# Kernel tuning notes

Measured on AMD Instinct MI355X. Metric: run time of the kernel, lower is better.

The kernel has to match this reference:

```python
import jax, jax.numpy as jnp
import numpy as np

B = 4; IN_CH = 256; HEAD_CH = 64; NUM_CLS = 3; H = 128; W = 128
NH = 4; KEY = 16; VAL = 16; OUT_CH = 2
VX = 0.1 * 8; VY = 0.1 * 8  # voxel_size[:2] * out_size_factor
DW = 1.6; DL = 3.9; STRIDE = 1
C_CTR = (HEAD_CH + 2 + NUM_CLS) * 9      # 621
C_COR = (HEAD_CH + 2 + NUM_CLS * 4) * 8  # 624
C_FG = (HEAD_CH + 2 + NUM_CLS) * 9       # 621


def _sampler_points():
    offs = np.arange(-STRIDE, STRIDE + 1, STRIDE, dtype=np.float32)
    oy, ox = np.meshgrid(offs, offs, indexing='ij')
    ctr = np.stack([ox, oy], 0).reshape(2, 9)  # pixel offsets
    cx = np.array([-DW/2, -DW/2, DW/2, DW/2, DL/2, -DL/2, DL/2, -DL/2], np.float32) / VX
    cy = np.array([DL/2, -DL/2, DL/2, -DL/2, -DW/2, -DW/2, DW/2, DW/2], np.float32) / VY
    # faithful to torch: stack(dim=1) -> [8,2] then .view(2,8) (row-major reinterpret)
    cor = np.stack([cx, cy], 1).reshape(2, 8)
    r = max(DW, DL)
    fx = np.array([-r/3, -r/3, -r/3, 0, 0, 0, r/3, r/3, r/3], np.float32) / VX
    fy = np.array([-r/3, 0, r/3, -r/3, 0, r/3, -r/3, 0, r/3], np.float32) / VY
    fg = np.stack([fx, fy], 1).reshape(2, 9)
    return jnp.asarray(ctr), jnp.asarray(cor), jnp.asarray(fg)


def _raw_grid():
    gx = jnp.arange(W, dtype=jnp.float32) + 0.5
    gy = jnp.arange(H, dtype=jnp.float32) + 0.5
    return jnp.stack([jnp.broadcast_to(gx[None, :], (H, W)),
                      jnp.broadcast_to(gy[:, None], (H, W))], 0)  # [2,H,W]


def _conv3x3(x, w, b):
    y = jax.lax.conv_general_dilated(x, w, (1, 1), 'SAME',
                                     dimension_numbers=('NCHW', 'OIHW', 'NCHW'))
    return y + b[None, :, None, None]


def _cbr3(x, w, b, s, t):  # conv3x3 + inference-mode BN (folded scale/shift) + relu
    return jax.nn.relu(_conv3x3(x, w, b) * s[None, :, None, None] + t[None, :, None, None])


def _cbr1(x, w, b, s, t):  # per-head 1x1 conv + BN + relu, w: [NH,O,C], x: [B,C,H,W]
    y = jnp.einsum('noc,bchw->nbohw', w, x) + b[:, None, :, None, None]
    return jax.nn.relu(y * s[:, None, :, None, None] + t[:, None, :, None, None])


def _sample(feats, grids):
    # feats [B,C,H,W]; grids [2,n,H,W] pixel coords. Matches F.grid_sample
    # (bilinear, zeros padding, align_corners=False): sample at pixel coord g-0.5.
    n = grids.shape[1]
    geo = jnp.stack([grids[0] / W, grids[1] / H], 0)  # recover_coords, [2,n,H,W]
    gx, gy = grids[0] - 0.5, grids[1] - 0.5
    x0f = jnp.floor(gx); y0f = jnp.floor(gy)
    dx, dy = gx - x0f, gy - y0f
    x0 = x0f.astype(jnp.int32); y0 = y0f.astype(jnp.int32)
    flat = feats.reshape(B, -1, H * W)

    def gather(xc, yc, wgt):
        valid = ((xc >= 0) & (xc < W) & (yc >= 0) & (yc < H)).astype(feats.dtype) * wgt
        idx = jnp.clip(yc, 0, H - 1) * W + jnp.clip(xc, 0, W - 1)
        v = jnp.take(flat, idx.reshape(-1), axis=2).reshape(B, -1, n, H, W)
        return v * valid[None, None]

    s = (gather(x0, y0, (1 - dx) * (1 - dy)) + gather(x0 + 1, y0, dx * (1 - dy))
         + gather(x0, y0 + 1, (1 - dx) * dy) + gather(x0 + 1, y0 + 1, dx * dy))
    geo_b = jnp.broadcast_to(geo[None], (B,) + geo.shape)
    out = jnp.concatenate([s, geo_b], axis=1)  # [B,C+2,n,H,W]
    return out.reshape(B, -1, H, W)           # channel index = c*n + p, as torch .view


def _forward(base_feats, cc_w, cc_b, cc_s, cc_t, ch_w, ch_b,
             oc_w, oc_b, oc_s, oc_t, oh_w, oh_b,
             fc_w, fc_b, fc_s, fc_t, fh_w, fh_b,
             q_w, q_b, q_s, q_t,
             ck_w, ck_b, ck_s, ck_t, cv_w, cv_b, cv_s, cv_t,
             kk_w, kk_b, kk_s, kk_t, kv_w, kv_b, kv_s, kv_t,
             fk_w, fk_b, fk_s, fk_t, fv_w, fv_b, fv_s, fv_t,
             p1_w, p1_b, p1_s, p1_t, p2_w, p2_b):
    center_feat = _cbr3(base_feats, cc_w, cc_b, cc_s, cc_t)
    center_map = _conv3x3(center_feat, ch_w, ch_b)
    corner_feat = _cbr3(base_feats, oc_w, oc_b, oc_s, oc_t)
    corner_map = _conv3x3(corner_feat, oh_w, oh_b)
    fg_feat = _cbr3(base_feats, fc_w, fc_b, fc_s, fc_t)
    fg_map = _conv3x3(fg_feat, fh_w, fh_b)

    ctr_pts, cor_pts, fg_pts = _sampler_points()
    raw = _raw_grid()
    g_ctr = raw[:, None] + ctr_pts[:, :, None, None]  # [2,9,H,W]
    g_cor = raw[:, None] + cor_pts[:, :, None, None]  # [2,8,H,W]
    g_fg = raw[:, None] + fg_pts[:, :, None, None]    # [2,9,H,W]

    cs = _sample(jnp.concatenate([center_feat, center_map], 1), g_ctr)  # [B,621,H,W]
    os_ = _sample(jnp.concatenate([corner_feat, corner_map], 1), g_cor)  # [B,624,H,W]
    fs = _sample(jnp.concatenate([fg_feat, fg_map], 1), g_fg)            # [B,621,H,W]

    q = _cbr1(base_feats, q_w, q_b, q_s, q_t)  # [NH,B,KEY,H,W]
    ck = _cbr1(cs, ck_w, ck_b, ck_s, ck_t); cv = _cbr1(cs, cv_w, cv_b, cv_s, cv_t)
    ok = _cbr1(os_, kk_w, kk_b, kk_s, kk_t); ov = _cbr1(os_, kv_w, kv_b, kv_s, kv_t)
    fk = _cbr1(fs, fk_w, fk_b, fk_s, fk_t); fv = _cbr1(fs, fv_w, fv_b, fv_s, fv_t)

    logits = jnp.stack([(q * ck).sum(2), (q * ok).sum(2), (q * fk).sum(2)], axis=2)  # [NH,B,3,H,W]
    attw = jax.nn.softmax(logits, axis=2)
    vals = jnp.stack([cv, ov, fv], axis=2)          # [NH,B,3,VAL,H,W]
    att = (attw[:, :, :, None] * vals).sum(2)       # [NH,B,VAL,H,W]

    # predict: 1x1 conv over cat([base_feats, att]) + BN + relu, then 1x1 to out_ch
    h1 = (jnp.einsum('noc,bchw->nbohw', p1_w[:, :, :IN_CH], base_feats)
          + jnp.einsum('nov,nbvhw->nbohw', p1_w[:, :, IN_CH:], att)
          + p1_b[:, None, :, None, None])
    h1 = jax.nn.relu(h1 * p1_s[:, None, :, None, None] + p1_t[:, None, :, None, None])
    pred = jnp.einsum('npo,nbohw->nbphw', p2_w, h1) + p2_b[:, None, :, None, None]
    heads = jnp.moveaxis(pred, 0, 1).reshape(B, NH * OUT_CH, H, W)
    return jnp.concatenate([center_map, corner_map, fg_map, heads], axis=1)  # [B,26,H,W]


def setup_inputs() -> dict:
    ks = iter(jax.random.split(jax.random.key(0), 80))

    def rn(shape, s=0.05):
        return jax.random.normal(next(ks), shape, jnp.float32) * s

    d = {"base_feats": jax.random.normal(next(ks), (B, IN_CH, H, W), jnp.float32)}
    for conv, head, hc in (("cc", "ch", NUM_CLS), ("oc", "oh", NUM_CLS * 4), ("fc", "fh", NUM_CLS)):
        d[conv + "_w"] = rn((HEAD_CH, IN_CH, 3, 3)); d[conv + "_b"] = rn((HEAD_CH,))
        d[conv + "_s"] = 1.0 + rn((HEAD_CH,)); d[conv + "_t"] = rn((HEAD_CH,))
        d[head + "_w"] = rn((hc, HEAD_CH, 3, 3)); d[head + "_b"] = jnp.full((hc,), -2.19, jnp.float32)
    d["q_w"] = rn((NH, KEY, IN_CH)); d["q_b"] = rn((NH, KEY))
    d["q_s"] = 1.0 + rn((NH, KEY)); d["q_t"] = rn((NH, KEY))
    for name, cin, cout in (("ck", C_CTR, KEY), ("cv", C_CTR, VAL), ("kk", C_COR, KEY),
                            ("kv", C_COR, VAL), ("fk", C_FG, KEY), ("fv", C_FG, VAL)):
        d[name + "_w"] = rn((NH, cout, cin)); d[name + "_b"] = rn((NH, cout))
        d[name + "_s"] = 1.0 + rn((NH, cout)); d[name + "_t"] = rn((NH, cout))
    d["p1_w"] = rn((NH, HEAD_CH, IN_CH + VAL)); d["p1_b"] = rn((NH, HEAD_CH))
    d["p1_s"] = 1.0 + rn((NH, HEAD_CH)); d["p1_t"] = rn((NH, HEAD_CH))
    d["p2_w"] = rn((NH, OUT_CH, HEAD_CH)); d["p2_b"] = jnp.full((NH, OUT_CH), -2.19, jnp.float32)
    return d


def reference(base_feats, cc_w, cc_b, cc_s, cc_t, ch_w, ch_b,
              oc_w, oc_b, oc_s, oc_t, oh_w, oh_b,
              fc_w, fc_b, fc_s, fc_t, fh_w, fh_b,
              q_w, q_b, q_s, q_t,
              ck_w, ck_b, ck_s, ck_t, cv_w, cv_b, cv_s, cv_t,
              kk_w, kk_b, kk_s, kk_t, kv_w, kv_b, kv_s, kv_t,
              fk_w, fk_b, fk_s, fk_t, fv_w, fv_b, fv_s, fv_t,
              p1_w, p1_b, p1_s, p1_t, p2_w, p2_b):
    return _forward(base_feats, cc_w, cc_b, cc_s, cc_t, ch_w, ch_b,
                    oc_w, oc_b, oc_s, oc_t, oh_w, oh_b,
                    fc_w, fc_b, fc_s, fc_t, fh_w, fh_b,
                    q_w, q_b, q_s, q_t,
                    ck_w, ck_b, ck_s, ck_t, cv_w, cv_b, cv_s, cv_t,
                    kk_w, kk_b, kk_s, kk_t, kv_w, kv_b, kv_s, kv_t,
                    fk_w, fk_b, fk_s, fk_t, fv_w, fv_b, fv_s, fv_t,
                    p1_w, p1_b, p1_s, p1_t, p2_w, p2_b)
```

## Files before the change

### kernel.cpp

```cpp
#include <hip/hip_runtime.h>
#include <hip/hip_bf16.h>
#include <math.h>


#define HW 16384
#define WIMG 128

typedef unsigned short ushortT;
typedef __attribute__((ext_vector_type(8))) short short8;
typedef __attribute__((ext_vector_type(4))) float floatx4;
typedef __attribute__((ext_vector_type(4))) unsigned uintx4;

constexpr size_t OFF_KV    = 16777216;
constexpr size_t OFF_A16   = 29360128;
constexpr size_t OFF_B16   = 38012928;
constexpr size_t OFF_CWT   = 46057216;
constexpr size_t OFF_CB    = OFF_CWT + 221184;
constexpr size_t OFF_HWT   = OFF_CB + 192;
constexpr size_t OFF_QWT   = OFF_HWT + 13824;
constexpr size_t OFF_QB    = OFF_QWT + 8192;
constexpr size_t OFF_KVW   = OFF_QB + 64;
constexpr size_t OFF_GEO   = OFF_KVW + 266240;
constexpr size_t OFF_P1WT  = OFF_GEO + 1152;
constexpr size_t OFF_P1B   = OFF_P1WT + 40960;

struct P53 { const float* p[53]; };

__device__ inline ushortT f2bf(float f) {
    unsigned u = __float_as_uint(f);
    unsigned r = (u + 0x7FFFu + ((u >> 16) & 1u)) >> 16;
    return (ushortT)r;
}
__device__ inline unsigned packbf(float a, float b) {
    return (unsigned)f2bf(a) | ((unsigned)f2bf(b) << 16);
}
__device__ inline float bf2f(ushortT u) {
    return __uint_as_float((unsigned)u << 16);
}

typedef __attribute__((address_space(3))) ushortT lds_us;
typedef __attribute__((address_space(1))) const ushortT glb_us;
__device__ inline void gload_lds16(const ushortT* g, ushortT* ldsbase) {
    __builtin_amdgcn_global_load_lds((glb_us*)g, (lds_us*)ldsbase, 16, 0, 0);
}

__device__ const float c_ox[3][9] = {
    {-1.f, 0.f, 1.f, -1.f, 0.f, 1.f, -1.f, 0.f, 1.f},
    {-1.f, 2.4375f, -1.f, -2.4375f, 1.f, 2.4375f, 1.f, -2.4375f, 0.f},
    {-1.625f, -1.625f, -1.625f, 0.f, -1.625f, 1.625f, 0.f, -1.625f, 0.f}};
__device__ const float c_oy[3][9] = {
    {-1.f, -1.f, -1.f, 0.f, 0.f, 0.f, 1.f, 1.f, 1.f},
    {2.4375f, -1.f, -2.4375f, -1.f, 2.4375f, 1.f, -2.4375f, 1.f, 0.f},
    {0.f, 0.f, 1.625f, 1.625f, -1.625f, 1.625f, 0.f, 1.625f, 1.625f}};

__device__ const int tapX_cor[16] = {-1,-1, 2, 3,-1,-1,-3,-2, 1, 1, 2, 3, 1, 1,-3,-2};
__device__ const int tapY_cor[16] = { 2, 3,-1,-1,-3,-2,-1,-1, 2, 3, 1, 1,-3,-2, 1, 1};
__device__ const int tapR_cor[16] = { 4, 5, 2, 2, 0, 1, 2, 2, 4, 5, 3, 3, 0, 1, 3, 3};

__device__ inline float cornw(float off, int X) {
    float f = floorf(off);
    float d = off - f;
    int fi = (int)f;
    return (X == fi) ? (1.f - d) : (X == fi + 1) ? d : 0.f;
}

__global__ __launch_bounds__(256) void setup_kernel(P53 ptrs, float* __restrict__ ws,
                                                    const float* __restrict__ base,
                                                    ushortT* __restrict__ a16,
                                                    ushortT* __restrict__ b16) {
    int i = blockIdx.x * 256 + threadIdx.x;
    const float* const* p = ptrs.p;
    if (i < 1102464) {
        if (i < 442368) {
            int tap = i / 49152, r = i % 49152;
            int g = r / 1536, r2 = r % 1536;
            int M = r2 >> 3, j = r2 & 7;
            int br = M >> 6, oc = M & 63, ic = g * 8 + j;
            float v = p[1 + 6 * br][(oc * 256 + ic) * 9 + tap] * p[3 + 6 * br][oc];
            ((ushortT*)(ws + OFF_CWT))[i] = f2bf(v);
            return;
        }
        i -= 442368;
        if (i < 192) {
            int br = i >> 6, oc = i & 63;
            ws[OFF_CB + i] = p[2 + 6 * br][oc] * p[3 + 6 * br][oc] + p[4 + 6 * br][oc];
            return;
        }
        i -= 192;
        if (i < 27648) {
            int j = i & 7, m = (i >> 3) & 15, u = (i >> 7) % 72, br = i / 9216;
            int cnt = (br == 1) ? 12 : 3;
            int t = u >> 3, g = u & 7, ic = g * 8 + j;
            const float* hw = (br == 0) ? p[5] : (br == 1) ? p[11] : p[17];
            float v = (m < cnt) ? hw[(m * 64 + ic) * 9 + t] : 0.f;
            ((ushortT*)(ws + OFF_HWT))[i] = f2bf(v);
            return;
        }
        i -= 27648;
        if (i < 16384) {
            int j = i & 7, m = (i >> 3) & 63, sg = i >> 9;
            int k = (sg >> 2) * 32 + (sg & 3) * 8 + j;
            ((ushortT*)(ws + OFF_QWT))[i] = f2bf(p[19][m * 256 + k] * p[21][m]);
            return;
        }
        i -= 16384;
        if (i < 64) { ws[OFF_QB + i] = p[20][i] * p[21][i] + p[22][i]; return; }
        i -= 64;
        if (i < 532480) {
            int br, NQ, NTAP, n, C, i2;
            if (i < 110592)      { br = 0; NQ = 3; NTAP = 9;  n = 9; C = 67; i2 = i; }
            else if (i < 274432) { br = 1; NQ = 4; NTAP = 16; n = 8; C = 76; i2 = i - 110592; }
            else                 { br = 2; NQ = 7; NTAP = 25; n = 9; C = 67; i2 = i - 274432; }
            int gsz = NQ * 4096;
            int g = i2 / gsz, r = i2 % gsz;
            int q = r >> 12, r2 = r & 4095;
            int sub = r2 >> 10, m = (r2 >> 3) & 127, j = r2 & 7;
            int t = q * 4 + sub, c = g * 8 + j;
            float v = 0.f;
            if (t < NTAP && c < C) {
                int X, Y;
                if (br == 0)      { X = t % 3 - 1; Y = t / 3 - 1; }
                else if (br == 1) { X = tapX_cor[t]; Y = tapY_cor[t]; }
                else              { X = t % 5 - 2; Y = t / 5 - 2; }
                const float* wsrc = (m < 64) ? p[23 + 8 * br] : p[27 + 8 * br];
                int mo = (m < 64) ? m : m - 64;
                float sc = (m < 64) ? p[25 + 8 * br][mo] : p[29 + 8 * br][mo];
                int Cn = (C + 2) * n;
                float s = 0.f;
                for (int pp = 0; pp < n; ++pp) {
                    float ww = cornw(c_ox[br][pp], X) * cornw(c_oy[br][pp], Y);
                    if (ww != 0.f) s += ww * wsrc[mo * Cn + c * n + pp];
                }
                v = s * sc;
            }
            ((ushortT*)(ws + OFF_KVW))[i] = f2bf(v);
            return;
        }
        i -= 532480;
        if (i < 1152) {
            int br = i / 384, rem = i % 384, which = rem >> 7, m = rem & 127;
            int n = (br == 1) ? 8 : 9, C = (br == 1) ? 76 : 67, Cn = (C + 2) * n;
            const float* wsrc = (m < 64) ? p[23 + 8 * br] : p[27 + 8 * br];
            int mo = (m < 64) ? m : m - 64;
            float sc = (m < 64) ? p[25 + 8 * br][mo] : p[29 + 8 * br][mo];
            float bb = (m < 64) ? p[24 + 8 * br][mo] : p[28 + 8 * br][mo];
            float tt = (m < 64) ? p[26 + 8 * br][mo] : p[30 + 8 * br][mo];
            float v = 0.f;
            if (which == 0) {
                for (int pp = 0; pp < n; ++pp) v += wsrc[mo * Cn + C * n + pp];
                v *= sc;
            } else if (which == 1) {
                for (int pp = 0; pp < n; ++pp) v += wsrc[mo * Cn + (C + 1) * n + pp];
                v *= sc;
            } else {
                for (int pp = 0; pp < n; ++pp)
                    v += wsrc[mo * Cn + C * n + pp] * c_ox[br][pp]
                       + wsrc[mo * Cn + (C + 1) * n + pp] * c_oy[br][pp];
                v = v * sc * 0.0078125f + bb * sc + tt;
            }
            ws[OFF_GEO + br * 384 + which * 128 + m] = v;
            return;
        }
        i -= 1152;
        if (i < 81920) {
            int j = i & 7, M = (i >> 3) & 255, sg = i >> 11;
            int k = (sg >> 2) * 32 + (sg & 3) * 8 + j;
            int nh = M >> 6, oc = M & 63;
            float sc = p[49][nh * 64 + oc];
            float v;
            if (k < 256) v = p[47][(nh * 64 + oc) * 272 + k] * sc;
            else {
                int k2 = k - 256, nh2 = k2 >> 4, va = k2 & 15;
                v = (nh2 == nh) ? p[47][(nh * 64 + oc) * 272 + 256 + va] * sc : 0.f;
            }
            ((ushortT*)(ws + OFF_P1WT))[i] = f2bf(v);
            return;
        }
        i -= 81920;
        if (i < 256) { ws[OFF_P1B + i] = p[48][i] * p[49][i] + p[50][i]; }
        return;
    }
    int idx = i - 1102464;
    if (idx < 4 * 32 * 130 * 130) {
        int col = idx % 130, t = idx / 130;
        int row = t % 130; t /= 130;
        int icg = t & 31, b = t >> 5;
        int h = row - 1, w = col - 1;
        unsigned wds[4] = {0u, 0u, 0u, 0u};
        if ((unsigned)h < 128u && (unsigned)w < 128u) {
            const float* s = base + (size_t)(b * 256 + icg * 8) * HW + h * WIMG + w;
            #pragma unroll
            for (int jp = 0; jp < 4; ++jp)
                wds[jp] = packbf(s[(size_t)(2 * jp) * HW], s[(size_t)(2 * jp + 1) * HW]);
        }
        unsigned* d = (unsigned*)(a16 + (size_t)idx * 8);
        d[0] = wds[0]; d[1] = wds[1]; d[2] = wds[2]; d[3] = wds[3];
        return;
    }
    idx -= 4 * 32 * 130 * 130;
    if (idx < 4 * 28 * 134 * 134) {
        int col = idx % 134, row = (idx / 134) % 134;
        if (row < 3 || row >= 131 || col < 3 || col >= 131) {
            unsigned* d = (unsigned*)(b16 + (size_t)idx * 8);
            d[0] = 0u; d[1] = 0u; d[2] = 0u; d[3] = 0u;
        }
    }
}

__global__ __launch_bounds__(256) void conv_base_mfma(
    const ushortT* __restrict__ a16, const ushortT* __restrict__ wA,
    const float* __restrict__ cb, ushortT* __restrict__ b16)
{
    const int wv = threadIdx.x >> 6, lane = threadIdx.x & 63;
    const int sub = lane >> 4, ln = lane & 15;
    const int xh = blockIdx.x, h = blockIdx.y, b = blockIdx.z;
    const int x0 = xh * 64;
    __shared__ __align__(16) ushortT sbuf[2][792 * 8];

    floatx4 acc[3][4];
    #pragma unroll
    for (int mt = 0; mt < 3; ++mt)
        #pragma unroll
        for (int nt = 0; nt < 4; ++nt)
            #pragma unroll
            for (int r = 0; r < 4; ++r) acc[mt][nt][r] = 0.f;

    const int wbase = threadIdx.x & ~63;
    auto stage = [&](int s, int buf) {
        #pragma unroll
        for (int it = 0; it < 4; ++it) {
            int idx = threadIdx.x + it * 256;
            if (idx < 792) {
                int col = idx % 66, t2 = idx / 66;
                int r = t2 % 3, icg = t2 / 3;
                const ushortT* g = a16 +
                    (((size_t)(b * 32 + s * 4 + icg) * 130 + (h + r)) * 130 + (x0 + col)) * 8;
                gload_lds16(g, &sbuf[buf][(size_t)(it * 256 + wbase) * 8]);
            }
        }
    };
    stage(0, 0);
    for (int s = 0; s < 8; ++s) {
        __syncthreads();
        if (s < 7) stage(s + 1, (s + 1) & 1);
        const ushortT* sb = sbuf[s & 1];
        #pragma unroll
        for (int tap = 0; tap < 9; ++tap) {
            const int ky = tap / 3, kx = tap % 3;
            short8 Bf[4];
            #pragma unroll
            for (int nt = 0; nt < 4; ++nt) {
                int c = nt * 16 + ln + kx;
                Bf[nt] = *(const short8*)(sb + ((sub * 3 + ky) * 66 + c) * 8);
            }
            const int g = s * 4 + sub;
            short8 Af[3];
            #pragma unroll
            for (int mt = 0; mt < 3; ++mt) {
                int m = wv * 48 + mt * 16 + ln;
                Af[mt] = *(const short8*)(wA + (((size_t)tap * 32 + g) * 192 + m) * 8);
            }
            #pragma unroll
            for (int mt = 0; mt < 3; ++mt)
                #pragma unroll
                for (int nt = 0; nt < 4; ++nt)
                    acc[mt][nt] = __builtin_amdgcn_mfma_f32_16x16x32_bf16(
                        Af[mt], Bf[nt], acc[mt][nt], 0, 0, 0);
        }
    }
    #pragma unroll
    for (int mt = 0; mt < 3; ++mt) {
        int ocq = wv * 48 + mt * 16 + sub * 4;
        #pragma unroll
        for (int nt = 0; nt < 4; ++nt) {
            int px = x0 + nt * 16 + ln;
            float v0 = fmaxf(acc[mt][nt][0] + cb[ocq + 0], 0.f);
            float v1 = fmaxf(acc[mt][nt][1] + cb[ocq + 1], 0.f);
            float v2 = fmaxf(acc[mt][nt][2] + cb[ocq + 2], 0.f);
            float v3 = fmaxf(acc[mt][nt][3] + cb[ocq + 3], 0.f);
            unsigned lo = packbf(v0, v1), hi = packbf(v2, v3);
            unsigned plo = (unsigned)__shfl_down((int)lo, 16);
            unsigned phi = (unsigned)__shfl_down((int)hi, 16);
            if (!(sub & 1)) {
                int br = ocq >> 6, oc = ocq & 63;
                int grp = ((br == 0) ? 0 : (br == 1) ? 9 : 19) + (oc >> 3);
                uintx4 w = {lo, hi, plo, phi};
                *(uintx4*)(b16 +
                    (((size_t)(b * 28 + grp) * 134 + (h + 3)) * 134 + (px + 3)) * 8) = w;
            }
        }
    }
}

__global__ __launch_bounds__(256) void conv_head_mfma(
    const ushortT* __restrict__ b16c, const ushortT* __restrict__ wH,
    const float* __restrict__ chb, const float* __restrict__ ohb,
    const float* __restrict__ fhb, float* __restrict__ out,
    ushortT* __restrict__ b16)
{
    const int wv = threadIdx.x >> 6, lane = threadIdx.x & 63;
    const int sub = lane >> 4, ln = lane & 15;
    const int h = blockIdx.x;
    const int br = blockIdx.y % 3, b = blockIdx.y / 3;
    const int cnt = (br == 1) ? 12 : 3;
    const int mapb = (br == 0) ? 0 : (br == 1) ? 3 : 15;
    const int grpb = (br == 0) ? 0 : (br == 1) ? 9 : 19;
    const float* bias = (br == 0) ? chb : (br == 1) ? ohb : fhb;
    __shared__ __align__(16) ushortT sbuf[8 * 3 * 130 * 8];
    const int wbase = threadIdx.x & ~63;

    for (int it = 0; it < 13; ++it) {
        int idx = threadIdx.x + it * 256;
        if (idx < 3120) {
            int col = idx % 130, t2 = idx / 130;
            int r = t2 % 3, g = t2 / 3;
            const ushortT* gp = b16c +
                (((size_t)(b * 28 + grpb + g) * 134 + (h + r + 2)) * 134 + (col + 2)) * 8;
            gload_lds16(gp, sbuf + (size_t)(it * 256 + wbase) * 8);
        }
    }
    __syncthreads();

    floatx4 acc[2];
    #pragma unroll
    for (int nt = 0; nt < 2; ++nt)
        #pragma unroll
        for (int r = 0; r < 4; ++r) acc[nt][r] = 0.f;
    #pragma unroll
    for (int k = 0; k < 18; ++k) {
        int u = k * 4 + sub;
        int t = u >> 3, g = u & 7;
        int dxv = t % 3 - 1, ry = t / 3;
        short8 Af = *(const short8*)(wH + ((size_t)(br * 72 + u) * 16 + ln) * 8);
        #pragma unroll
        for (int nt = 0; nt < 2; ++nt) {
            int c = wv * 32 + nt * 16 + ln + dxv + 1;
            short8 Bf = *(const short8*)(sbuf + ((g * 3 + ry) * 130 + c) * 8);
            acc[nt] = __builtin_amdgcn_mfma_f32_16x16x32_bf16(Af, Bf, acc[nt], 0, 0, 0);
        }
    }
    #pragma unroll
    for (int nt = 0; nt < 2; ++nt) {
        int px = wv * 32 + nt * 16 + ln;
        #pragma unroll
        for (int r = 0; r < 4; ++r) {
            int m = sub * 4 + r;
            if (m < cnt) {
                float v = acc[nt][r] + bias[m];
                out[((size_t)b * 26 + mapb + m) * HW + h * WIMG + px] = v;
                int grp = grpb + 8 + (m >> 3), j = m & 7;
                b16[(((size_t)(b * 28 + grp) * 134 + (h + 3)) * 134 + (px + 3)) * 8 + j]
                    = f2bf(v);
            }
        }
    }
}

template<int BRV>
__global__ __launch_bounds__(256, 6) void kv_grp(
    const ushortT* __restrict__ b16, const ushortT* __restrict__ kvw,
    const float* __restrict__ geob, ushortT* __restrict__ kvout)
{
    constexpr int NG    = (BRV == 0) ? 9  : (BRV == 1) ? 10 : 9;
    constexpr int NTAP  = (BRV == 0) ? 9  : (BRV == 1) ? 16 : 25;
    constexpr int NQ    = (BRV == 0) ? 3  : (BRV == 1) ? 4  : 7;
    constexpr int ROWS  = (BRV == 0) ? 3  : (BRV == 1) ? 6  : 5;
    constexpr int COLS  = (BRV == 0) ? 66 : (BRV == 1) ? 70 : 68;
    constexpr int XMIN  = (BRV == 0) ? -1 : (BRV == 1) ? -3 : -2;
    constexpr int UBASE = (BRV == 0) ? 0  : (BRV == 1) ? 9  : 19;
    constexpr int NEL   = ROWS * COLS;
    constexpr int NIT   = (NEL + 255) / 256;
    constexpr int WBASE = (BRV == 0) ? 0 : (BRV == 1) ? 110592 : 274432;

    const int lane = threadIdx.x & 63, wv = threadIdx.x >> 6;
    const int sub = lane >> 4, ln = lane & 15;
    const int mw = wv >> 1, nw = wv & 1;
    const int x0 = blockIdx.x * 64, h = blockIdx.y;
    const int b = blockIdx.z;

    __shared__ __align__(16) ushortT sbuf[2][NEL * 8];
    const int wbase = threadIdx.x & ~63;
    const int thrB = (nw * 32 + ln) * 16;

    int boff[NQ];
    #pragma unroll
    for (int q = 0; q < NQ; ++q) {
        int t = q * 4 + sub;
        int dxv, ry;
        if (t >= NTAP)          { dxv = -XMIN; ry = 0; }
        else if (BRV == 0)      { dxv = t % 3 - 1; ry = t / 3; }
        else if (BRV == 1)      { dxv = tapX_cor[t]; ry = tapR_cor[t]; }
        else                    { dxv = t % 5 - 2; ry = t / 5; }
        boff[q] = (ry * COLS + (dxv - XMIN)) * 16 + thrB;
    }

    auto stage = [&](int g, int buf) {
        #pragma unroll
        for (int it = 0; it < NIT; ++it) {
            int idx = threadIdx.x + it * 256;
            if (idx < NEL) {
                int rw = idx / COLS, col = idx % COLS;
                int dy = (BRV == 1) ? ((rw < 3) ? rw - 3 : rw - 2) : (rw - ROWS / 2);
                const ushortT* gp = b16 +
                    (((size_t)(b * 28 + UBASE + g) * 134 + (h + dy + 3)) * 134
                     + (x0 + col + XMIN + 3)) * 8;
                gload_lds16(gp, &sbuf[buf][(size_t)(it * 256 + wbase) * 8]);
            }
        }
    };

    floatx4 acc[4][2];
    #pragma unroll
    for (int mt = 0; mt < 4; ++mt)
        #pragma unroll
        for (int nt = 0; nt < 2; ++nt)
            #pragma unroll
            for (int r = 0; r < 4; ++r) acc[mt][nt][r] = 0.f;

    const ushortT* wp0 = kvw + WBASE + (size_t)sub * 1024 + (mw * 64 + ln) * 8;

    stage(0, 0);
    __syncthreads();
    int cur = 0;
    for (int g = 0; g < NG; ++g) {
        const char* sb8 = (const char*)sbuf[cur];
        const ushortT* wg = wp0 + (size_t)g * (NQ * 4096);
        short8 A0[4], B0[2], A1[4], B1[2];
        auto ldf = [&](int q, short8 A[4], short8 B[2]) {
            const ushortT* wp = wg + (size_t)q * 4096;
            #pragma unroll
            for (int mt = 0; mt < 4; ++mt)
                A[mt] = *(const short8*)(wp + mt * 128);
            int bb = boff[q];
            #pragma unroll
            for (int nt = 0; nt < 2; ++nt)
                B[nt] = *(const short8*)(sb8 + bb + nt * 256);
        };
        auto dom = [&](short8 A[4], short8 B[2]) {
            #pragma unroll
            for (int mt = 0; mt < 4; ++mt)
                #pragma unroll
                for (int nt = 0; nt < 2; ++nt)
                    acc[mt][nt] = __builtin_amdgcn_mfma_f32_16x16x32_bf16(
                        A[mt], B[nt], acc[mt][nt], 0, 0, 0);
        };
        ldf(0, A0, B0);
        if (g + 1 < NG) stage(g + 1, cur ^ 1);
        #pragma unroll
        for (int q = 0; q < NQ; q += 2) {
            bool h1 = (q + 1 < NQ);
            if (h1) ldf(q + 1, A1, B1);
            dom(A0, B0);
            if (q + 2 < NQ) ldf(q + 2, A0, B0);
            if (h1) dom(A1, B1);
        }
        __syncthreads();
        cur ^= 1;
    }

    const float* geo = geob + BRV * 384;
    const float fy = (h + 0.5f) * 0.0078125f;
    #pragma unroll
    for (int mt = 0; mt < 4; ++mt)
        #pragma unroll
        for (int nt = 0; nt < 2; ++nt) {
            int px = x0 + nw * 32 + nt * 16 + ln;
            float fx = (px + 0.5f) * 0.0078125f;
            #pragma unroll
            for (int r = 0; r < 4; ++r) {
                int Mi = mw * 64 + mt * 16 + sub * 4 + r;
                float v = acc[mt][nt][r] + geo[Mi] * fx + geo[128 + Mi] * fy + geo[256 + Mi];
                kvout[((size_t)(BRV * 4 + b) * 128 + Mi) * HW + h * WIMG + px] =
                    f2bf(fmaxf(v, 0.f));
            }
        }
}

__global__ __launch_bounds__(256) void attn_pred_mfma(
    float* __restrict__ ws, const float* __restrict__ p2w,
    const float* __restrict__ p2b, float* __restrict__ out)
{
    const int wv = threadIdx.x >> 6, lane = threadIdx.x & 63;
    const int sub = lane >> 4, ln = lane & 15;
    const int px0 = blockIdx.x * 64, b = blockIdx.y;
    const ushortT* wP1 = (const ushortT*)(ws + OFF_P1WT);
    const ushortT* wQ  = (const ushortT*)(ws + OFF_QWT);
    const ushortT* a16 = (const ushortT*)(ws + OFF_A16);
    const ushortT* kv = (const ushortT*)(ws + OFF_KV);
    const float* p1b = ws + OFF_P1B;
    const float* qb  = ws + OFF_QB;
    __shared__ __align__(16) ushortT xbuf[40 * 64 * 8];
    __shared__ __align__(16) ushortT qld[64 * 64];

    const int mypx = threadIdx.x & 63, nh = threadIdx.x >> 6;
    const int gpx = px0 + mypx, hh = gpx >> 7, ww = gpx & 127;
    #pragma unroll
    for (int g2 = 0; g2 < 8; ++g2) {
        int g = nh * 8 + g2;
        const ushortT* gp = a16 +
            (((size_t)(b * 32 + g) * 130 + (hh + 1)) * 130 + (ww + 1)) * 8;
        gload_lds16(gp, xbuf + (size_t)g * 64 * 8);
    }
    __syncthreads();

    {
        floatx4 qacc[4];
        #pragma unroll
        for (int nt = 0; nt < 4; ++nt)
            #pragma unroll
            for (int r = 0; r < 4; ++r) qacc[nt][r] = 0.f;
        #pragma unroll
        for (int kk = 0; kk < 8; ++kk) {
            short8 Af = *(const short8*)(wQ + (((kk * 4 + sub) * 64) + wv * 16 + ln) * 8);
            #pragma unroll
            for (int nt = 0; nt < 4; ++nt) {
                short8 Bf = *(const short8*)(xbuf + (((kk * 4 + sub) * 64) + nt * 16 + ln) * 8);
                qacc[nt] = __builtin_amdgcn_mfma_f32_16x16x32_bf16(Af, Bf, qacc[nt], 0, 0, 0);
            }
        }
        #pragma unroll
        for (int nt = 0; nt < 4; ++nt)
            #pragma unroll
            for (int r = 0; r < 4; ++r) {
                int row = wv * 16 + sub * 4 + r;
                qld[row * 64 + nt * 16 + ln] = f2bf(fmaxf(qacc[nt][r] + qb[row], 0.f));
            }
    }
    __syncthreads();

    {
        float l[3];
        #pragma unroll
        for (int br = 0; br < 3; ++br) {
            float s = 0.f;
            #pragma unroll
            for (int ko = 0; ko < 16; ++ko)
                s = fmaf(bf2f(qld[(nh * 16 + ko) * 64 + mypx]),
                         bf2f(kv[(size_t)((br * 4 + b) * 128 + nh * 16 + ko) * HW + gpx]), s);
            l[br] = s;
        }
        float m = fmaxf(l[0], fmaxf(l[1], l[2]));
        float e0 = __expf(l[0] - m), e1 = __expf(l[1] - m), e2 = __expf(l[2] - m);
        float inv = 1.f / (e0 + e1 + e2);
        float aw0 = e0 * inv, aw1 = e1 * inv, aw2 = e2 * inv;
        #pragma unroll
        for (int vap = 0; vap < 8; ++vap) {
            int va0 = vap * 2, va1 = vap * 2 + 1;
            float a0 =
                aw0 * bf2f(kv[(size_t)((0 * 4 + b) * 128 + 64 + nh * 16 + va0) * HW + gpx]) +
                aw1 * bf2f(kv[(size_t)((1 * 4 + b) * 128 + 64 + nh * 16 + va0) * HW + gpx]) +
                aw2 * bf2f(kv[(size_t)((2 * 4 + b) * 128 + 64 + nh * 16 + va0) * HW + gpx]);
            float a1 =
                aw0 * bf2f(kv[(size_t)((0 * 4 + b) * 128 + 64 + nh * 16 + va1) * HW + gpx]) +
                aw1 * bf2f(kv[(size_t)((1 * 4 + b) * 128 + 64 + nh * 16 + va1) * HW + gpx]) +
                aw2 * bf2f(kv[(size_t)((2 * 4 + b) * 128 + 64 + nh * 16 + va1) * HW + gpx]);
            int g = 32 + nh * 2 + (vap >> 2), wo = vap & 3;
            ((unsigned*)xbuf)[(g * 64 + mypx) * 4 + wo] = packbf(a0, a1);
        }
    }
    __syncthreads();

    floatx4 acc[4][4];
    #pragma unroll
    for (int mt = 0; mt < 4; ++mt)
        #pragma unroll
        for (int nt = 0; nt < 4; ++nt)
            #pragma unroll
            for (int r = 0; r < 4; ++r) acc[mt][nt][r] = 0.f;
    #pragma unroll
    for (int kk = 0; kk < 10; ++kk) {
        short8 Bf[4];
        #pragma unroll
        for (int nt = 0; nt < 4; ++nt)
            Bf[nt] = *(const short8*)(xbuf + (((kk * 4 + sub) * 64) + nt * 16 + ln) * 8);
        #pragma unroll
        for (int mt = 0; mt < 4; ++mt) {
            short8 Af = *(const short8*)(wP1 +
                (((size_t)(kk * 4 + sub) * 256) + wv * 64 + mt * 16 + ln) * 8);
            #pragma unroll
            for (int nt = 0; nt < 4; ++nt)
                acc[mt][nt] = __builtin_amdgcn_mfma_f32_16x16x32_bf16(Af, Bf[nt], acc[mt][nt], 0, 0, 0);
        }
    }

    float po0[4] = {0.f, 0.f, 0.f, 0.f}, po1[4] = {0.f, 0.f, 0.f, 0.f};
    #pragma unroll
    for (int mt = 0; mt < 4; ++mt)
        #pragma unroll
        for (int r = 0; r < 4; ++r) {
            int oc = mt * 16 + sub * 4 + r;
            float bias = p1b[wv * 64 + oc];
            float w0 = p2w[(wv * 2 + 0) * 64 + oc];
            float w1 = p2w[(wv * 2 + 1) * 64 + oc];
            #pragma unroll
            for (int nt = 0; nt < 4; ++nt) {
                float hv = fmaxf(acc[mt][nt][r] + bias, 0.f);
                po0[nt] = fmaf(w0, hv, po0[nt]);
                po1[nt] = fmaf(w1, hv, po1[nt]);
            }
        }
    #pragma unroll
    for (int nt = 0; nt < 4; ++nt) {
        po0[nt] += __shfl_xor(po0[nt], 16);
        po0[nt] += __shfl_xor(po0[nt], 32);
        po1[nt] += __shfl_xor(po1[nt], 16);
        po1[nt] += __shfl_xor(po1[nt], 32);
    }
    if (sub == 0) {
        #pragma unroll
        for (int nt = 0; nt < 4; ++nt) {
            int px = px0 + nt * 16 + ln;
            out[((size_t)b * 26 + 18 + wv * 2 + 0) * HW + px] = po0[nt] + p2b[wv * 2 + 0];
            out[((size_t)b * 26 + 18 + wv * 2 + 1) * HW + px] = po1[nt] + p2b[wv * 2 + 1];
        }
    }
}

extern "C" void kernel_launch(void* const* d_in, const int* in_sizes, int n_in,
                              void* d_out, int out_size, void* d_ws, size_t ws_size,
                              hipStream_t stream) {
    (void)in_sizes; (void)n_in; (void)out_size; (void)ws_size;
    float* ws  = (float*)d_ws;
    float* out = (float*)d_out;
    const float* base = (const float*)d_in[0];
    P53 ptrs;
    for (int i = 0; i < 53; ++i) ptrs.p[i] = (const float*)d_in[i];

    ushortT* a16 = (ushortT*)(ws + OFF_A16);
    ushortT* b16 = (ushortT*)(ws + OFF_B16);
    ushortT* kvb = (ushortT*)(ws + OFF_KV);
    const ushortT* kvw = (const ushortT*)(ws + OFF_KVW);

    setup_kernel<<<20613, 256, 0, stream>>>(ptrs, ws, base, a16, b16);
    conv_base_mfma<<<dim3(2, 128, 4), 256, 0, stream>>>(
        a16, (const ushortT*)(ws + OFF_CWT), ws + OFF_CB, b16);
    conv_head_mfma<<<dim3(128, 12), 256, 0, stream>>>(
        b16, (const ushortT*)(ws + OFF_HWT),
        (const float*)d_in[6], (const float*)d_in[12], (const float*)d_in[18],
        out, b16);
    kv_grp<0><<<dim3(2, 128, 4), 256, 0, stream>>>(b16, kvw, ws + OFF_GEO, kvb);
    kv_grp<1><<<dim3(2, 128, 4), 256, 0, stream>>>(b16, kvw, ws + OFF_GEO, kvb);
    kv_grp<2><<<dim3(2, 128, 4), 256, 0, stream>>>(b16, kvw, ws + OFF_GEO, kvb);
    attn_pred_mfma<<<dim3(256, 4), 256, 0, stream>>>(ws, (const float*)d_in[51],
                                                     (const float*)d_in[52], out);
}
```

Before: 460.4 us.

## Merge three kv_grp launches into one kernel and halve conv_head tile width

The three per-branch kv_grp launches are folded into a single kv_all2 kernel that dispatches on blockIdx.z to a templated device body and shares one LDS buffer sized for the largest branch (420 elements). This removes two launch boundaries and lets blocks from different branches overlap on the GPU, at the cost of every block reserving the largest branch's LDS footprint. Separately, conv_head_mfma now processes 64-pixel half rows per block (twice as many blocks, one MFMA tile per wave) to improve parallelism and reduce LDS per block.

After: 450.3 us. 2.2% less time.

```diff
diff --git a/kernel.cpp b/kernel.cpp
--- a/kernel.cpp
+++ b/kernel.cpp
@@ -300,53 +300,47 @@
 {
     const int wv = threadIdx.x >> 6, lane = threadIdx.x & 63;
     const int sub = lane >> 4, ln = lane & 15;
-    const int h = blockIdx.x;
+    const int x0 = (blockIdx.x & 1) * 64, h = blockIdx.x >> 1;
     const int br = blockIdx.y % 3, b = blockIdx.y / 3;
     const int cnt = (br == 1) ? 12 : 3;
     const int mapb = (br == 0) ? 0 : (br == 1) ? 3 : 15;
     const int grpb = (br == 0) ? 0 : (br == 1) ? 9 : 19;
     const float* bias = (br == 0) ? chb : (br == 1) ? ohb : fhb;
-    __shared__ __align__(16) ushortT sbuf[8 * 3 * 130 * 8];
+    __shared__ __align__(16) ushortT sbuf[8 * 3 * 66 * 8];
     const int wbase = threadIdx.x & ~63;
 
-    for (int it = 0; it < 13; ++it) {
+    for (int it = 0; it < 7; ++it) {
         int idx = threadIdx.x + it * 256;
-        if (idx < 3120) {
-            int col = idx % 130, t2 = idx / 130;
+        if (idx < 1584) {
+            int col = idx % 66, t2 = idx / 66;
             int r = t2 % 3, g = t2 / 3;
             const ushortT* gp = b16c +
-                (((size_t)(b * 28 + grpb + g) * 134 + (h + r + 2)) * 134 + (col + 2)) * 8;
+                (((size_t)(b * 28 + grpb + g) * 134 + (h + r + 2)) * 134 + (x0 + col + 2)) * 8;
             gload_lds16(gp, sbuf + (size_t)(it * 256 + wbase) * 8);
         }
     }
     __syncthreads();
 
-    floatx4 acc[2];
-    #pragma unroll
-    for (int nt = 0; nt < 2; ++nt)
-        #pragma unroll
-        for (int r = 0; r < 4; ++r) acc[nt][r] = 0.f;
+    floatx4 acc;
+    #pragma unroll
+    for (int r = 0; r < 4; ++r) acc[r] = 0.f;
     #pragma unroll
     for (int k = 0; k < 18; ++k) {
         int u = k * 4 + sub;
         int t = u >> 3, g = u & 7;
         int dxv = t % 3 - 1, ry = t / 3;
         short8 Af = *(const short8*)(wH + ((size_t)(br * 72 + u) * 16 + ln) * 8);
-        #pragma unroll
-        for (int nt = 0; nt < 2; ++nt) {
-            int c = wv * 32 + nt * 16 + ln + dxv + 1;
-            short8 Bf = *(const short8*)(sbuf + ((g * 3 + ry) * 130 + c) * 8);
-            acc[nt] = __builtin_amdgcn_mfma_f32_16x16x32_bf16(Af, Bf, acc[nt], 0, 0, 0);
-        }
-    }
-    #pragma unroll
-    for (int nt = 0; nt < 2; ++nt) {
-        int px = wv * 32 + nt * 16 + ln;
+        int c = wv * 16 + ln + dxv + 1;
+        short8 Bf = *(const short8*)(sbuf + ((g * 3 + ry) * 66 + c) * 8);
+        acc = __builtin_amdgcn_mfma_f32_16x16x32_bf16(Af, Bf, acc, 0, 0, 0);
+    }
+    {
+        int px = x0 + wv * 16 + ln;
         #pragma unroll
         for (int r = 0; r < 4; ++r) {
             int m = sub * 4 + r;
             if (m < cnt) {
-                float v = acc[nt][r] + bias[m];
+                float v = acc[r] + bias[m];
                 out[((size_t)b * 26 + mapb + m) * HW + h * WIMG + px] = v;
                 int grp = grpb + 8 + (m >> 3), j = m & 7;
                 b16[(((size_t)(b * 28 + grp) * 134 + (h + 3)) * 134 + (px + 3)) * 8 + j]
@@ -357,9 +351,10 @@
 }
 
 template<int BRV>
-__global__ __launch_bounds__(256, 6) void kv_grp(
+__device__ __forceinline__ void kv_body(
     const ushortT* __restrict__ b16, const ushortT* __restrict__ kvw,
-    const float* __restrict__ geob, ushortT* __restrict__ kvout)
+    const float* __restrict__ geob, ushortT* __restrict__ kvout,
+    ushortT* __restrict__ sbufRaw)
 {
     constexpr int NG    = (BRV == 0) ? 9  : (BRV == 1) ? 10 : 9;
     constexpr int NTAP  = (BRV == 0) ? 9  : (BRV == 1) ? 16 : 25;
@@ -376,9 +371,8 @@
     const int sub = lane >> 4, ln = lane & 15;
     const int mw = wv >> 1, nw = wv & 1;
     const int x0 = blockIdx.x * 64, h = blockIdx.y;
-    const int b = blockIdx.z;
-
-    __shared__ __align__(16) ushortT sbuf[2][NEL * 8];
+    const int b = blockIdx.z & 3;
+
     const int wbase = threadIdx.x & ~63;
     const int thrB = (nw * 32 + ln) * 16;
 
@@ -404,7 +398,8 @@
                 const ushortT* gp = b16 +
                     (((size_t)(b * 28 + UBASE + g) * 134 + (h + dy + 3)) * 134
                      + (x0 + col + XMIN + 3)) * 8;
-                gload_lds16(gp, &sbuf[buf][(size_t)(it * 256 + wbase) * 8]);
+                gload_lds16(gp, sbufRaw + (size_t)buf * (NEL * 8)
+                                        + (size_t)(it * 256 + wbase) * 8);
             }
         }
     };
@@ -423,7 +418,7 @@
     __syncthreads();
     int cur = 0;
     for (int g = 0; g < NG; ++g) {
-        const char* sb8 = (const char*)sbuf[cur];
+        const char* sb8 = (const char*)(sbufRaw + (size_t)cur * (NEL * 8));
         const ushortT* wg = wp0 + (size_t)g * (NQ * 4096);
         short8 A0[4], B0[2], A1[4], B1[2];
         auto ldf = [&](int q, short8 A[4], short8 B[2]) {
@@ -474,6 +469,17 @@
                     f2bf(fmaxf(v, 0.f));
             }
         }
+}
+
+__global__ __launch_bounds__(256, 6) void kv_all2(
+    const ushortT* __restrict__ b16, const ushortT* __restrict__ kvw,
+    const float* __restrict__ geob, ushortT* __restrict__ kvout)
+{
+    __shared__ __align__(16) ushortT sbuf[2 * 420 * 8];
+    const int brv = blockIdx.z >> 2;
+    if (brv == 0)      kv_body<0>(b16, kvw, geob, kvout, sbuf);
+    else if (brv == 1) kv_body<1>(b16, kvw, geob, kvout, sbuf);
+    else               kv_body<2>(b16, kvw, geob, kvout, sbuf);
 }
 
 __global__ __launch_bounds__(256) void attn_pred_mfma(
@@ -634,13 +640,11 @@
     setup_kernel<<<20613, 256, 0, stream>>>(ptrs, ws, base, a16, b16);
     conv_base_mfma<<<dim3(2, 128, 4), 256, 0, stream>>>(
         a16, (const ushortT*)(ws + OFF_CWT), ws + OFF_CB, b16);
-    conv_head_mfma<<<dim3(128, 12), 256, 0, stream>>>(
+    conv_head_mfma<<<dim3(256, 12), 256, 0, stream>>>(
         b16, (const ushortT*)(ws + OFF_HWT),
         (const float*)d_in[6], (const float*)d_in[12], (const float*)d_in[18],
         out, b16);
-    kv_grp<0><<<dim3(2, 128, 4), 256, 0, stream>>>(b16, kvw, ws + OFF_GEO, kvb);
-    kv_grp<1><<<dim3(2, 128, 4), 256, 0, stream>>>(b16, kvw, ws + OFF_GEO, kvb);
-    kv_grp<2><<<dim3(2, 128, 4), 256, 0, stream>>>(b16, kvw, ws + OFF_GEO, kvb);
+    kv_all2<<<dim3(2, 128, 12), 256, 0, stream>>>(b16, kvw, ws + OFF_GEO, kvb);
     attn_pred_mfma<<<dim3(256, 4), 256, 0, stream>>>(ws, (const float*)d_in[51],
                                                      (const float*)d_in[52], out);
 }
```
